# Kernel optimization log

Measured on AMD Instinct MI355X. Metric: run time of the kernel, lower is better.

## Reference

```python
import jax, jax.numpy as jnp
import numpy as np

B, T, D = 64, 1024, 1024  # batch, seq_len, in_dim == out_dim
N_UNIT = 2


def _lstm_cell(x, h, c, Wih, Whh):
    # x:[B,Din], h,c:[B,D]; Wih:[4D,Din], Whh:[4D,D]  (PyTorch gate order i,f,g,o)
    gates = x @ Wih.T + h @ Whh.T           # [B,4D]
    i, f, g, o = jnp.split(gates, 4, axis=-1)
    i = jax.nn.sigmoid(i)
    f = jax.nn.sigmoid(f)
    g = jnp.tanh(g)
    o = jax.nn.sigmoid(o)
    c_new = f * c + i * g
    h_new = o * jnp.tanh(c_new)
    return h_new, c_new


def setup_inputs() -> dict:
    key = jax.random.key(0)
    ks = jax.random.split(key, 5)
    s_in = 1.0 / np.sqrt(D)
    x = jax.random.normal(ks[0], (B, T, D), dtype=jnp.float32)
    Wih0 = jax.random.normal(ks[1], (4 * D, D), dtype=jnp.float32) * s_in
    Whh0 = jax.random.normal(ks[2], (4 * D, D), dtype=jnp.float32) * s_in
    Wih1 = jax.random.normal(ks[3], (4 * D, D), dtype=jnp.float32) * s_in
    Whh1 = jax.random.normal(ks[4], (4 * D, D), dtype=jnp.float32) * s_in
    return {"x": x, "Wih0": Wih0, "Whh0": Whh0, "Wih1": Wih1, "Whh1": Whh1}


def reference(x, Wih0, Whh0, Wih1, Whh1):
    b = x.shape[0]
    d = Whh0.shape[1]
    z = jnp.zeros((b, d), dtype=x.dtype)
    # Original code seeds both h and c of every unit with the same zeros tensor.
    carry0 = (z, z, z, z)  # (h0, c0, h1, c1)

    def step(carry, xt):
        h0, c0, h1, c1 = carry
        h0, c0 = _lstm_cell(xt, h0, c0, Wih0, Whh0)
        h1, c1 = _lstm_cell(h0, h1, c1, Wih1, Whh1)
        return (h0, c0, h1, c1), h1

    xs = jnp.swapaxes(x, 0, 1)  # [T,B,D]
    _, outs = jax.lax.scan(step, carry0, xs)
    return jnp.swapaxes(outs, 0, 1)  # [B,T,D]
```

## Files before the change

kernel.cpp:

```cpp
#include <hip/hip_runtime.h>
#include <cstdint>
#include <cstddef>

#define B_ 64
#define T_ 1024
#define D_ 1024
#define NBLK 256

typedef __attribute__((ext_vector_type(8))) _Float16 half8;
typedef __attribute__((ext_vector_type(4))) float f32x4;
typedef unsigned int u32;
typedef unsigned long long u64;
typedef unsigned short u16;

static __device__ __forceinline__ f32x4 mfma16(half8 a, half8 b, f32x4 c) {
  return __builtin_amdgcn_mfma_f32_16x16x32_f16(a, b, c, 0, 0, 0);
}
static __device__ __forceinline__ u64 cohl64(const u64* p) {
  return __hip_atomic_load(p, __ATOMIC_RELAXED, __HIP_MEMORY_SCOPE_AGENT);
}
static __device__ __forceinline__ u32 cohl32(const u32* p) {
  return __hip_atomic_load(p, __ATOMIC_RELAXED, __HIP_MEMORY_SCOPE_AGENT);
}
static __device__ __forceinline__ void cohs32(u32* p, u32 v) {
  __hip_atomic_store(p, v, __ATOMIC_RELAXED, __HIP_MEMORY_SCOPE_AGENT);
}
static __device__ __forceinline__ u16 h2u(_Float16 h) {
  return __builtin_bit_cast(u16, h);
}


static __device__ __forceinline__ void stage_coh(const _Float16* src, u64* st, int tid) {
  const int r = tid >> 5, j = tid & 31;
  const u64* p0 = (const u64*)(src + (size_t)r * D_) + j * 2;
  const u64* p1 = (const u64*)(src + (size_t)(r + 16) * D_) + j * 2;
  #pragma unroll
  for (int k = 0; k < 4; ++k) {
    st[2 * k] = cohl64(p0 + k * 64);
    st[2 * k + 1] = cohl64(p0 + k * 64 + 1);
    st[8 + 2 * k] = cohl64(p1 + k * 64);
    st[8 + 2 * k + 1] = cohl64(p1 + k * 64 + 1);
  }
}
static __device__ __forceinline__ void stage_x(const _Float16* src, u64* st, int tid) {
  const int r = tid >> 5, j = tid & 31;
  const u64* p0 = (const u64*)(src + (size_t)r * T_ * D_) + j * 2;
  const u64* p1 = (const u64*)(src + (size_t)(r + 16) * T_ * D_) + j * 2;
  #pragma unroll
  for (int k = 0; k < 4; ++k) {
    st[2 * k] = p0[k * 64];
    st[2 * k + 1] = p0[k * 64 + 1];
    st[8 + 2 * k] = p1[k * 64];
    st[8 + 2 * k + 1] = p1[k * 64 + 1];
  }
}
static __device__ __forceinline__ void stage_xf(const float* src, u64* st, int tid) {
  const int r = tid >> 5, j = tid & 31;
  #pragma unroll
  for (int h = 0; h < 2; ++h) {
    const float4* p = (const float4*)(src + (size_t)(r + h * 16) * T_ * D_) + j * 2;
    #pragma unroll
    for (int k = 0; k < 4; ++k) {
      #pragma unroll
      for (int q = 0; q < 2; ++q) {
        float4 v = p[k * 64 + q];
        union { u16 us[4]; u64 u; } pk;
        pk.us[0] = h2u((_Float16)v.x); pk.us[1] = h2u((_Float16)v.y);
        pk.us[2] = h2u((_Float16)v.z); pk.us[3] = h2u((_Float16)v.w);
        st[h * 8 + 2 * k + q] = pk.u;
      }
    }
  }
}
static __device__ __forceinline__ void stage_write(char* lds, const u64* st, int tid) {
  const int r = tid >> 5, j = tid & 31;
  #pragma unroll
  for (int h = 0; h < 2; ++h) {
    const int rr = r + h * 16;
    const int sw = (rr & 7) << 4;
    char* row = lds + rr * 2048;
    #pragma unroll
    for (int k = 0; k < 4; ++k) {
      char* dst = row + ((j * 16 + k * 512) ^ sw);
      *(u64*)dst = st[h * 8 + 2 * k];
      *(u64*)(dst + 8) = st[h * 8 + 2 * k + 1];
    }
  }
}

static __device__ __forceinline__ void gemm_gp(
    f32x4* acc, const char* ldsA, const half8* wA, const half8* wBv,
    int kq, int lane) {
  const int r = lane & 15;
  const int kl2 = (lane >> 4) << 4;
  const int sw = (r & 7) << 4;
  const char* p0 = ldsA + r * 2048;
  const char* p1 = ldsA + (16 + r) * 2048;
  #pragma unroll
  for (int ks = 0; ks < 8; ++ks) {
    const int kb = (kq * 512 + ks * 64 + kl2) ^ sw;
    half8 a0 = *(const half8*)(p0 + kb);
    half8 a1 = *(const half8*)(p1 + kb);
    acc[0] = mfma16(a0, wA[ks], acc[0]);
    acc[1] = mfma16(a1, wA[ks], acc[1]);
    acc[2] = mfma16(a0, wBv[ks], acc[2]);
    acc[3] = mfma16(a1, wBv[ks], acc[3]);
  }
}

static __device__ __forceinline__ void pollwait2(const u32* slots, u32 gen0,
                                                 u32 gen1, int tid) {
  if (tid < NBLK) {
    const u32 tgt = (tid < 128) ? gen0 : gen1;
    if (tgt > 0) {
      const u32* p = slots + tid * 32;
      int spin = 0;
      while (cohl32(p) < tgt && ++spin < (1 << 16))
        __builtin_amdgcn_s_sleep(2);
    }
  }
  __syncthreads();
}


template <bool XPRE>
__global__ __launch_bounds__(512, 2) void lstm_persist(
    const float* __restrict__ x32, const _Float16* __restrict__ xh,
    const _Float16* __restrict__ W,
    _Float16* h0,
    _Float16* h1,
    float* __restrict__ out, u32* slots)
{
  __shared__ char ldsA[32 * 2048];
  __shared__ float glp[4][32][68];
  const int tid = threadIdx.x;
  const int lane = tid & 63;
  const int wv = tid >> 6;
  const int kq = wv >> 1;
  const int gp = wv & 1;
  const int bid = blockIdx.x;
  const int slot = bid >> 3;
  const int lyr = slot >> 4;
  const int mh = (slot >> 3) & 1;
  const int dgrp = (bid & 7) * 8 + (slot & 7);
  const int d0 = dgrp << 4;
  const int mbase = mh << 5;
  const int r = lane & 15;
  const int klane = lane >> 4;

  const _Float16* Wih = W + (size_t)(2 * lyr) * 4096 * 1024;
  const _Float16* Whh = Wih + (size_t)4096 * 1024;
  const size_t row0 = (size_t)((gp * 2) * 1024 + d0 + r) * 1024 + kq * 256 + klane * 8;
  const size_t row1 = (size_t)((gp * 2 + 1) * 1024 + d0 + r) * 1024 + kq * 256 + klane * 8;
  half8 wihA[8], wihB[8], whhA[8], whhB[8];
  #pragma unroll
  for (int ks = 0; ks < 8; ++ks) {
    wihA[ks] = *(const half8*)(Wih + row0 + ks * 32);
    wihB[ks] = *(const half8*)(Wih + row1 + ks * 32);
    whhA[ks] = *(const half8*)(Whh + row0 + ks * 32);
    whhB[ks] = *(const half8*)(Whh + row1 + ks * 32);
  }
  #pragma unroll
  for (int ks = 0; ks < 8; ++ks) {
    asm volatile("" : "+v"(wihA[ks]));
    asm volatile("" : "+v"(wihB[ks]));
    asm volatile("" : "+v"(whhA[ks]));
    asm volatile("" : "+v"(whhB[ks]));
  }

  float creg0 = 0.f, creg1 = 0.f;
  const int cb = tid >> 3;
  const int cd = (tid & 7) << 1;
  const size_t HS = (size_t)B_ * D_;

  u64 st[16];
  if (lyr == 0) {
    if (XPRE) stage_x(xh + (size_t)mbase * T_ * D_, st, tid);
    else      stage_xf(x32 + (size_t)mbase * T_ * D_, st, tid);
  }

  for (int s = 0; s <= T_; ++s) {
    const bool active = lyr ? (s >= 1) : (s < T_);
    const int t = lyr ? (s - 1) : s;

    if (lyr == 0)
      pollwait2(slots, (u32)s, (u32)(s > 4 ? s - 4 : 0), tid);
    else
      pollwait2(slots, (u32)s, (u32)s, tid);

    if (active) {
      const _Float16* h0prev = h0 + (size_t)((s + 7) & 7) * HS + (size_t)mbase * D_;
      if (lyr == 0) {
        stage_write(ldsA, st, tid);
        __syncthreads();
        stage_coh(h0prev, st, tid);
      } else {
        stage_coh(h0prev, st, tid);
        stage_write(ldsA, st, tid);
        __syncthreads();
        stage_coh(h1 + (size_t)(s & 1) * HS + (size_t)mbase * D_, st, tid);
      }

      f32x4 acc[4];
      #pragma unroll
      for (int i = 0; i < 4; ++i) acc[i] = (f32x4){0.f, 0.f, 0.f, 0.f};
      gemm_gp(acc, ldsA, wihA, wihB, kq, lane);
      __syncthreads();
      stage_write(ldsA, st, tid);
      __syncthreads();
      gemm_gp(acc, ldsA, whhA, whhB, kq, lane);

      {
        const int r4 = klane << 2;
        const int c0 = (gp * 2) * 16 + r;
        #pragma unroll
        for (int i = 0; i < 4; ++i) {
          glp[kq][r4 + i][c0]           = acc[0][i];
          glp[kq][16 + r4 + i][c0]      = acc[1][i];
          glp[kq][r4 + i][c0 + 16]      = acc[2][i];
          glp[kq][16 + r4 + i][c0 + 16] = acc[3][i];
        }
      }
      __syncthreads();

      if (tid < 256) {
        float g4[4][2];
        #pragma unroll
        for (int gg = 0; gg < 4; ++gg) {
          g4[gg][0] = glp[0][cb][gg * 16 + cd] + glp[1][cb][gg * 16 + cd]
                    + glp[2][cb][gg * 16 + cd] + glp[3][cb][gg * 16 + cd];
          g4[gg][1] = glp[0][cb][gg * 16 + cd + 1] + glp[1][cb][gg * 16 + cd + 1]
                    + glp[2][cb][gg * 16 + cd + 1] + glp[3][cb][gg * 16 + cd + 1];
        }
        const float i0 = 1.f / (1.f + expf(-g4[0][0])), i1 = 1.f / (1.f + expf(-g4[0][1]));
        const float f0 = 1.f / (1.f + expf(-g4[1][0])), f1 = 1.f / (1.f + expf(-g4[1][1]));
        const float z0 = tanhf(g4[2][0]),               z1 = tanhf(g4[2][1]);
        const float o0 = 1.f / (1.f + expf(-g4[3][0])), o1 = 1.f / (1.f + expf(-g4[3][1]));
        creg0 = f0 * creg0 + i0 * z0;
        creg1 = f1 * creg1 + i1 * z1;
        const float hn0 = o0 * tanhf(creg0);
        const float hn1 = o1 * tanhf(creg1);
        union { u16 us[2]; u32 u; } pk;
        pk.us[0] = h2u((_Float16)hn0);
        pk.us[1] = h2u((_Float16)hn1);
        _Float16* hw = lyr
            ? (h1 + (size_t)((s + 1) & 1) * HS)
            : (h0 + (size_t)(s & 7) * HS);
        cohs32((u32*)(hw + (size_t)(mbase + cb) * D_ + d0 + cd), pk.u);
        if (lyr) {
          float2 o2; o2.x = hn0; o2.y = hn1;
          *(float2*)(out + ((size_t)(mbase + cb) * T_ + t) * D_ + d0 + cd) = o2;
        }
      }
    }

    __syncthreads();
    if (tid == 0) cohs32(slots + bid * 32, (u32)(s + 1));

    if (lyr == 0 && s + 1 < T_) {
      if (XPRE) stage_x(xh + ((size_t)mbase * T_ + (s + 1)) * D_, st, tid);
      else      stage_xf(x32 + ((size_t)mbase * T_ + (s + 1)) * D_, st, tid);
    }
  }
}

__global__ void convw(const float* __restrict__ w0, const float* __restrict__ w1,
                      const float* __restrict__ w2, const float* __restrict__ w3,
                      u64* __restrict__ dst) {
  const size_t n1 = (size_t)D_ * D_;
  const size_t n = 4 * n1;
  for (size_t i = (size_t)blockIdx.x * blockDim.x + threadIdx.x; i < n;
       i += (size_t)gridDim.x * blockDim.x) {
    const size_t m = i / n1, j = i - m * n1;
    const float* src = (m == 0) ? w0 : (m == 1) ? w1 : (m == 2) ? w2 : w3;
    float4 v = ((const float4*)src)[j];
    union { u16 us[4]; u64 u; } pk;
    pk.us[0] = h2u((_Float16)v.x); pk.us[1] = h2u((_Float16)v.y);
    pk.us[2] = h2u((_Float16)v.z); pk.us[3] = h2u((_Float16)v.w);
    dst[i] = pk.u;
  }
}
__global__ void convx(const float* __restrict__ x, u64* __restrict__ xh) {
  const size_t n = (size_t)B_ * T_ * D_ / 4;
  for (size_t i = (size_t)blockIdx.x * blockDim.x + threadIdx.x; i < n;
       i += (size_t)gridDim.x * blockDim.x) {
    float4 v = ((const float4*)x)[i];
    union { u16 us[4]; u64 u; } pk;
    pk.us[0] = h2u((_Float16)v.x); pk.us[1] = h2u((_Float16)v.y);
    pk.us[2] = h2u((_Float16)v.z); pk.us[3] = h2u((_Float16)v.w);
    xh[i] = pk.u;
  }
}

extern "C" void kernel_launch(void* const* d_in, const int* in_sizes, int n_in,
                              void* d_out, int out_size, void* d_ws, size_t ws_size,
                              hipStream_t stream) {
  (void)in_sizes; (void)n_in; (void)out_size;
  const float* x = (const float*)d_in[0];
  const float* Wih0 = (const float*)d_in[1];
  const float* Whh0 = (const float*)d_in[2];
  const float* Wih1 = (const float*)d_in[3];
  const float* Whh1 = (const float*)d_in[4];
  float* out = (float*)d_out;

  char* ws = (char*)d_ws;
  const size_t MB = 1ull << 20;
  const size_t KB = 1024;
  _Float16* Wf = (_Float16*)ws;
  _Float16* h0 = (_Float16*)(ws + 32 * MB);
  _Float16* h1 = (_Float16*)(ws + 33 * MB);
  u32* slots = (u32*)(ws + 33 * MB + 256 * KB);
  _Float16* xh = (_Float16*)(ws + 35 * MB);
  const bool xpre = ws_size >= 35 * MB + (size_t)B_ * T_ * D_ * 2;

  hipMemsetAsync(ws + 32 * MB, 0, 1 * MB + 256 * KB + 32 * KB, stream);
  convw<<<4096, 256, 0, stream>>>(Wih0, Whh0, Wih1, Whh1, (u64*)Wf);
  if (xpre) {
    convx<<<4096, 256, 0, stream>>>(x, (u64*)xh);
    lstm_persist<true><<<NBLK, 512, 0, stream>>>(x, xh, Wf, h0, h1, out, slots);
  } else {
    lstm_persist<false><<<NBLK, 512, 0, stream>>>(x, xh, Wf, h0, h1, out, slots);
  }
}
```

Measured before the change: 5.778 ms.

## Replace flat all-block polling with two-level gatherer barrier and overlap x-GEMM before wait

Each group of 32 blocks now has one gatherer block that polls its members' slots and publishes a single per-group done counter. Every block waits on at most 8 group counters instead of polling 256 per-block slots. Layer 0 now runs its input-projection GEMM before waiting on the recurrent dependency, with separate LDS buffers so staging does not collide. This aims to cut cross-block barrier latency and hide part of it behind compute. The cost is an extra hop of latency through the gatherer block, and LDS use doubles to 128 KB per block, which may reduce occupancy.

```diff
diff --git a/kernel.cpp b/kernel.cpp
--- a/kernel.cpp
+++ b/kernel.cpp
@@ -108,14 +108,18 @@
   }
 }
 
-static __device__ __forceinline__ void pollwait2(const u32* slots, u32 gen0,
-                                                 u32 gen1, int tid) {
-  if (tid < NBLK) {
-    const u32 tgt = (tid < 128) ? gen0 : gen1;
+static __device__ __forceinline__ void treewait(const u32* done, int lyr,
+                                                int mh, int s, int tid) {
+  if (tid < 8) {
+    const int gl = tid >> 2;
+    const int gm = (tid >> 1) & 1;
+    u32 tgt = 0;
+    if (gm == mh)
+      tgt = (gl == lyr) ? (u32)s
+          : (lyr == 0) ? (u32)(s > 4 ? s - 4 : 0) : (u32)s;
     if (tgt > 0) {
-      const u32* p = slots + tid * 32;
       int spin = 0;
-      while (cohl32(p) < tgt && ++spin < (1 << 16))
+      while (cohl32(done + tid) < tgt && ++spin < (1 << 16))
         __builtin_amdgcn_s_sleep(2);
     }
   }
@@ -129,10 +133,12 @@
     const _Float16* __restrict__ W,
     _Float16* h0,
     _Float16* h1,
-    float* __restrict__ out, u32* slots)
+    float* __restrict__ out, u32* slots, u32* done)
 {
-  __shared__ char ldsA[32 * 2048];
-  __shared__ float glp[4][32][68];
+  __shared__ char bufA[65536];
+  __shared__ char bufB[65536];
+  float (*glp)[32][68] = (float (*)[32][68])bufA;
+
   const int tid = threadIdx.x;
   const int lane = tid & 63;
   const int wv = tid >> 6;
@@ -172,6 +178,8 @@
   const int cb = tid >> 3;
   const int cd = (tid & 7) << 1;
   const size_t HS = (size_t)B_ * D_;
+  const int g = bid >> 5;
+  const bool gatherer = (bid & 31) == 0;
 
   u64 st[16];
   if (lyr == 0) {
@@ -182,34 +190,40 @@
   for (int s = 0; s <= T_; ++s) {
     const bool active = lyr ? (s >= 1) : (s < T_);
     const int t = lyr ? (s - 1) : s;
-
-    if (lyr == 0)
-      pollwait2(slots, (u32)s, (u32)(s > 4 ? s - 4 : 0), tid);
-    else
-      pollwait2(slots, (u32)s, (u32)s, tid);
-
-    if (active) {
-      const _Float16* h0prev = h0 + (size_t)((s + 7) & 7) * HS + (size_t)mbase * D_;
-      if (lyr == 0) {
-        stage_write(ldsA, st, tid);
+    const _Float16* h0prev = h0 + (size_t)((s + 7) & 7) * HS + (size_t)mbase * D_;
+
+    f32x4 acc[4];
+    #pragma unroll
+    for (int i = 0; i < 4; ++i) acc[i] = (f32x4){0.f, 0.f, 0.f, 0.f};
+
+    if (lyr == 0) {
+      if (active) {
+        stage_write(bufA, st, tid);
         __syncthreads();
+        gemm_gp(acc, bufA, wihA, wihB, kq, lane);
+      }
+      treewait(done, 0, mh, s, tid);
+      if (active) {
         stage_coh(h0prev, st, tid);
-      } else {
+        stage_write(bufB, st, tid);
+        __syncthreads();
+        gemm_gp(acc, bufB, whhA, whhB, kq, lane);
+      }
+    } else {
+      treewait(done, 1, mh, s, tid);
+      if (active) {
         stage_coh(h0prev, st, tid);
-        stage_write(ldsA, st, tid);
+        stage_write(bufA, st, tid);
         __syncthreads();
         stage_coh(h1 + (size_t)(s & 1) * HS + (size_t)mbase * D_, st, tid);
-      }
-
-      f32x4 acc[4];
-      #pragma unroll
-      for (int i = 0; i < 4; ++i) acc[i] = (f32x4){0.f, 0.f, 0.f, 0.f};
-      gemm_gp(acc, ldsA, wihA, wihB, kq, lane);
-      __syncthreads();
-      stage_write(ldsA, st, tid);
-      __syncthreads();
-      gemm_gp(acc, ldsA, whhA, whhB, kq, lane);
-
+        gemm_gp(acc, bufA, wihA, wihB, kq, lane);
+        stage_write(bufB, st, tid);
+        __syncthreads();
+        gemm_gp(acc, bufB, whhA, whhB, kq, lane);
+      }
+    }
+
+    if (active) {
       {
         const int r4 = klane << 2;
         const int c0 = (gp * 2) * 16 + r;
@@ -257,6 +271,16 @@
     __syncthreads();
     if (tid == 0) cohs32(slots + bid * 32, (u32)(s + 1));
 
+    if (gatherer) {
+      if (tid < 32) {
+        const u32* p = slots + (g * 32 + tid) * 32;
+        int spin = 0;
+        while (cohl32(p) < (u32)(s + 1) && ++spin < (1 << 18))
+          __builtin_amdgcn_s_sleep(1);
+      }
+      if (tid == 0) cohs32(done + g, (u32)(s + 1));
+    }
+
     if (lyr == 0 && s + 1 < T_) {
       if (XPRE) stage_x(xh + ((size_t)mbase * T_ + (s + 1)) * D_, st, tid);
       else      stage_xf(x32 + ((size_t)mbase * T_ + (s + 1)) * D_, st, tid);
@@ -310,15 +334,16 @@
   _Float16* h0 = (_Float16*)(ws + 32 * MB);
   _Float16* h1 = (_Float16*)(ws + 33 * MB);
   u32* slots = (u32*)(ws + 33 * MB + 256 * KB);
+  u32* done = slots + 8192;
   _Float16* xh = (_Float16*)(ws + 35 * MB);
   const bool xpre = ws_size >= 35 * MB + (size_t)B_ * T_ * D_ * 2;
 
-  hipMemsetAsync(ws + 32 * MB, 0, 1 * MB + 256 * KB + 32 * KB, stream);
+  hipMemsetAsync(ws + 32 * MB, 0, 1 * MB + 256 * KB + 33 * KB, stream);
   convw<<<4096, 256, 0, stream>>>(Wih0, Whh0, Wih1, Whh1, (u64*)Wf);
   if (xpre) {
     convx<<<4096, 256, 0, stream>>>(x, (u64*)xh);
-    lstm_persist<true><<<NBLK, 512, 0, stream>>>(x, xh, Wf, h0, h1, out, slots);
+    lstm_persist<true><<<NBLK, 512, 0, stream>>>(x, xh, Wf, h0, h1, out, slots, done);
   } else {
-    lstm_persist<false><<<NBLK, 512, 0, stream>>>(x, xh, Wf, h0, h1, out, slots);
-  }
-}
+    lstm_persist<false><<<NBLK, 512, 0, stream>>>(x, xh, Wf, h0, h1, out, slots, done);
+  }
+}
```

Result: slower. 7.193 ms (+24.5%).
